# Kernel optimization log

Hardware: AMD Instinct MI355X
Metric: run time of the kernel (lower is better)

Reference implementation:

```python
import jax, jax.numpy as jnp
import numpy as np


def _bicubic_warp(img, dx, dy):
    """Faithful JAX port of Warp_Object.forward with flag='bicubic'.
    img: [B,C,H,W] float32; dx, dy: [B,1,H,W] pixel displacements.
    Replicates the original tile-order quirk: X/Y are repeated C times along
    dim0 (order c*B+b) while the image is flattened in b*C+c order.
    """
    B, C, H, W = img.shape
    Wm1 = jnp.float32(max(W - 1, 1))
    Hm1 = jnp.float32(max(H - 1, 1))
    xs = jnp.arange(W, dtype=jnp.float32)
    ys = jnp.arange(H, dtype=jnp.float32)
    Xg, Yg = jnp.meshgrid(xs, ys)          # [H,W]
    # normalized grid in [-1,1] as in forward()
    newX = 2.0 * (Xg[None] + dx[:, 0]) / Wm1 - 1.0   # [B,H,W]
    newY = 2.0 * (Yg[None] + dy[:, 0]) / Hm1 - 1.0
    # repeat over channels exactly like X.repeat([C,1,1,1]) (tile order)
    x_map = (jnp.tile(newX, (C, 1, 1)) + 1.0) * Wm1 / 2.0   # [B*C,H,W]
    y_map = (jnp.tile(newY, (C, 1, 1)) + 1.0) * Hm1 / 2.0

    x0 = jnp.floor(x_map)
    y0 = jnp.floor(y_map)
    tx = x_map - x0
    ty = y_map - y0

    def cubic_coeffs(t):
        cm1 = (-t ** 3 + 2.0 * t ** 2 - t) / 2.0
        c0 = (3.0 * t ** 3 - 5.0 * t ** 2 + 2.0) / 2.0
        c1 = (-3.0 * t ** 3 + 4.0 * t ** 2 + t) / 2.0
        c2 = 1.0 - (cm1 + c0 + c1)
        return (cm1, c0, c1, c2)

    cx = cubic_coeffs(tx)
    cy = cubic_coeffs(ty)

    x0i = x0.astype(jnp.int32)
    y0i = y0.astype(jnp.int32)
    xi = [jnp.clip(x0i + o, 0, W - 1) for o in (-1, 0, 1, 2)]
    yi = [jnp.clip(y0i + o, 0, H - 1) for o in (-1, 0, 1, 2)]

    flat = img.reshape(B * C, H, W)
    row = jnp.arange(B * C)[:, None, None]   # per-image base offset

    out = jnp.zeros_like(x_map)
    for j in range(4):            # 4 rows of the 4x4 bicubic stencil
        row_acc = jnp.zeros_like(x_map)
        for i in range(4):
            row_acc = row_acc + cx[i] * flat[row, yi[j], xi[i]]
        out = out + cy[j] * row_acc
    return out.reshape(B, C, H, W)


def setup_inputs() -> dict:
    key = jax.random.key(0)
    k1, k2, k3 = jax.random.split(key, 3)
    B, C, H, W = 4, 3, 512, 512
    input_image = jax.random.normal(k1, (B, C, H, W), dtype=jnp.float32)
    delta_x = jax.random.normal(k2, (B, 1, H, W), dtype=jnp.float32) * 1.5
    delta_y = jax.random.normal(k3, (B, 1, H, W), dtype=jnp.float32) * 1.5
    return {"input_image": input_image, "delta_x": delta_x, "delta_y": delta_y}


def reference(input_image, delta_x, delta_y):
    return _bicubic_warp(input_image, delta_x, delta_y)
```

## Files before the change

kernel.cpp:

```cpp
#include <hip/hip_runtime.h>


constexpr int B = 4, C = 3, H = 512, W = 512;
constexpr int HW = H * W;
constexpr int TH = 4;
constexpr int HALO_UP = 6, HALO_DN = 7;
constexpr int RS = TH + HALO_UP + HALO_DN;
constexpr int STRIDE = 516;
constexpr int NPOS = 4;
constexpr int NT = 512;
constexpr int NB = B * (H / TH);

typedef float f4 __attribute__((ext_vector_type(4)));
typedef f4 f4u __attribute__((aligned(4)));

__global__ __launch_bounds__(NT, 4)
void warp_bicubic_planes(const float* __restrict__ img,
                         const float* __restrict__ dxp,
                         const float* __restrict__ dyp,
                         float* __restrict__ out)
{
    __shared__ float tile[RS * STRIDE];

    int b   = blockIdx.x;
    int swz = (b & 7) * (NB / 8) + (b >> 3);
    int bd   = swz >> 7;
    int band = swz & 127;
    int yb   = band * TH;

    int tid  = threadIdx.x;
    int wave = tid >> 6;
    int ry   = wave >> 1;
    int half = wave & 1;
    int lane = tid & 63;
    int y    = yb + ry;
    int xbase = half * 256 + lane;

    const float* __restrict__ dxr = dxp + bd * HW + y * W + xbase;
    const float* __restrict__ dyr = dyp + bd * HW + y * W + xbase;
    float dxa[NPOS], dya[NPOS];
#pragma unroll
    for (int p = 0; p < NPOS; ++p) {
        dxa[p] = __builtin_nontemporal_load(dxr + 64 * p);
        dya[p] = __builtin_nontemporal_load(dyr + 64 * p);
    }

    float wx[NPOS][4];
    float cyw[NPOS][4];
    int   lbase[NPOS];
    unsigned relv[NPOS];
    int   sv[NPOS];
#pragma unroll
    for (int p = 0; p < NPOS; ++p) {
        int x = xbase + 64 * p;
        float xm = (float)x + dxa[p];
        float ym = (float)y + dya[p];
        float x0f = floorf(xm), y0f = floorf(ym);
        float tx = xm - x0f, ty = ym - y0f;
        int x0 = (int)x0f, y0 = (int)y0f;
        int s  = min(max(x0 - 1, 0), W - 4);
        sv[p] = s;

        float tx2 = tx * tx, tx3 = tx2 * tx;
        float cx0 = (-tx3 + 2.0f * tx2 - tx) * 0.5f;
        float cx1 = (3.0f * tx3 - 5.0f * tx2 + 2.0f) * 0.5f;
        float cx2 = (-3.0f * tx3 + 4.0f * tx2 + tx) * 0.5f;
        float cx3 = 1.0f - (cx0 + cx1 + cx2);

        float ty2 = ty * ty, ty3 = ty2 * ty;
        cyw[p][0] = (-ty3 + 2.0f * ty2 - ty) * 0.5f;
        cyw[p][1] = (3.0f * ty3 - 5.0f * ty2 + 2.0f) * 0.5f;
        cyw[p][2] = (-3.0f * ty3 + 4.0f * ty2 + ty) * 0.5f;
        cyw[p][3] = 1.0f - (cyw[p][0] + cyw[p][1] + cyw[p][2]);

        if (__builtin_expect(x0 >= 1 && x0 <= W - 3, 1)) {
            wx[p][0] = cx0; wx[p][1] = cx1; wx[p][2] = cx2; wx[p][3] = cx3;
        } else {
            float w0 = 0.f, w1 = 0.f, w2 = 0.f, w3 = 0.f;
            const float cxa[4] = {cx0, cx1, cx2, cx3};
#pragma unroll
            for (int o = 0; o < 4; ++o) {
                int xi = min(max(x0 - 1 + o, 0), W - 1);
                int e  = xi - s;
                float c = cxa[o];
                w0 += (e == 0) ? c : 0.f;
                w1 += (e == 1) ? c : 0.f;
                w2 += (e == 2) ? c : 0.f;
                w3 += (e == 3) ? c : 0.f;
            }
            wx[p][0] = w0; wx[p][1] = w1; wx[p][2] = w2; wx[p][3] = w3;
        }

        unsigned rel = (unsigned)(y0 - (yb - HALO_UP + 1));
        relv[p]  = rel;
        lbase[p] = (int)rel * STRIDE + s;
    }

#pragma unroll
    for (int c = 0; c < C; ++c) {
        int kp = bd + 4 * c;
        const float* __restrict__ plane = img + (size_t)kp * HW;

        if (c > 0) __syncthreads();
        for (int cc = tid; cc < RS * 128; cc += NT) {
            int r   = cc >> 7;
            int col = (cc & 127) << 2;
            int sr  = min(max(yb - HALO_UP + r, 0), H - 1);
            *(f4*)&tile[r * STRIDE + col] = *(const f4*)(plane + sr * W + col);
        }
        __syncthreads();

        float* __restrict__ orow = out + (size_t)kp * HW + y * W + xbase;
#pragma unroll
        for (int p = 0; p < NPOS; ++p) {
            float acc;
            if (__builtin_expect(relv[p] <= (unsigned)(RS - 4), 1)) {
                const float* rp = &tile[lbase[p]];
                float r0 = cyw[p][0] * (wx[p][0]*rp[0] + wx[p][1]*rp[1] + wx[p][2]*rp[2] + wx[p][3]*rp[3]);
                rp += STRIDE;
                float r1 = cyw[p][1] * (wx[p][0]*rp[0] + wx[p][1]*rp[1] + wx[p][2]*rp[2] + wx[p][3]*rp[3]);
                rp += STRIDE;
                float r2 = cyw[p][2] * (wx[p][0]*rp[0] + wx[p][1]*rp[1] + wx[p][2]*rp[2] + wx[p][3]*rp[3]);
                rp += STRIDE;
                float r3 = cyw[p][3] * (wx[p][0]*rp[0] + wx[p][1]*rp[1] + wx[p][2]*rp[2] + wx[p][3]*rp[3]);
                acc = (r0 + r1) + (r2 + r3);
            } else {
                int y0 = (int)relv[p] + (yb - HALO_UP + 1);
                acc = 0.f;
#pragma unroll
                for (int j = 0; j < 4; ++j) {
                    int yi = min(max(y0 - 1 + j, 0), H - 1);
                    f4 v = *(const f4u*)(plane + yi * W + sv[p]);
                    acc += cyw[p][j] * (wx[p][0]*v.x + wx[p][1]*v.y + wx[p][2]*v.z + wx[p][3]*v.w);
                }
            }
            __builtin_nontemporal_store(acc, orow + 64 * p);
        }
    }
}

extern "C" void kernel_launch(void* const* d_in, const int* in_sizes, int n_in,
                              void* d_out, int out_size, void* d_ws, size_t ws_size,
                              hipStream_t stream) {
    const float* img = (const float*)d_in[0];
    const float* dx  = (const float*)d_in[1];
    const float* dy  = (const float*)d_in[2];
    float* out = (float*)d_out;

    dim3 block(NT);
    dim3 grid(NB);
    hipLaunchKernelGGL(warp_bicubic_planes, grid, block, 0, stream,
                       img, dx, dy, out);
}
```

Baseline: 18.49 us.

## Split each row band into two x-halves with a narrower LDS tile

```diff
diff --git a/kernel.cpp b/kernel.cpp
--- a/kernel.cpp
+++ b/kernel.cpp
@@ -6,60 +6,60 @@
 constexpr int TH = 4;
 constexpr int HALO_UP = 6, HALO_DN = 7;
 constexpr int RS = TH + HALO_UP + HALO_DN;
-constexpr int STRIDE = 516;
-constexpr int NPOS = 4;
+constexpr int LST = 272;
+constexpr int NPOS = 2;
 constexpr int NT = 512;
-constexpr int NB = B * (H / TH);
+constexpr int NB = B * (H / TH) * 2;
 
 typedef float f4 __attribute__((ext_vector_type(4)));
 typedef f4 f4u __attribute__((aligned(4)));
 
-__global__ __launch_bounds__(NT, 4)
-void warp_bicubic_planes(const float* __restrict__ img,
+__global__ __launch_bounds__(NT, 8)
+void warp_bicubic_xsplit(const float* __restrict__ img,
                          const float* __restrict__ dxp,
                          const float* __restrict__ dyp,
                          float* __restrict__ out)
 {
-    __shared__ float tile[RS * STRIDE];
+    __shared__ float tile[RS * LST];
 
     int b   = blockIdx.x;
     int swz = (b & 7) * (NB / 8) + (b >> 3);
-    int bd   = swz >> 7;
-    int band = swz & 127;
+    int bd   = swz >> 8;
+    int band = (swz >> 1) & 127;
+    int half = swz & 1;
     int yb   = band * TH;
+    int xb   = half * 256;
+    int cb   = half ? 248 : 0;
 
     int tid  = threadIdx.x;
     int wave = tid >> 6;
     int ry   = wave >> 1;
-    int half = wave & 1;
+    int hw   = wave & 1;
     int lane = tid & 63;
     int y    = yb + ry;
-    int xbase = half * 256 + lane;
+    int xs   = xb + hw * 128 + lane;
+    int pixoff = y * W + xs;
 
-    const float* __restrict__ dxr = dxp + bd * HW + y * W + xbase;
-    const float* __restrict__ dyr = dyp + bd * HW + y * W + xbase;
     float dxa[NPOS], dya[NPOS];
 #pragma unroll
     for (int p = 0; p < NPOS; ++p) {
-        dxa[p] = __builtin_nontemporal_load(dxr + 64 * p);
-        dya[p] = __builtin_nontemporal_load(dyr + 64 * p);
+        dxa[p] = __builtin_nontemporal_load(dxp + bd * HW + pixoff + 64 * p);
+        dya[p] = __builtin_nontemporal_load(dyp + bd * HW + pixoff + 64 * p);
     }
 
     float wx[NPOS][4];
     float cyw[NPOS][4];
-    int   lbase[NPOS];
     unsigned relv[NPOS];
-    int   sv[NPOS];
+    unsigned lsv[NPOS];
 #pragma unroll
     for (int p = 0; p < NPOS; ++p) {
-        int x = xbase + 64 * p;
+        int x = xs + 64 * p;
         float xm = (float)x + dxa[p];
         float ym = (float)y + dya[p];
         float x0f = floorf(xm), y0f = floorf(ym);
         float tx = xm - x0f, ty = ym - y0f;
         int x0 = (int)x0f, y0 = (int)y0f;
         int s  = min(max(x0 - 1, 0), W - 4);
-        sv[p] = s;
 
         float tx2 = tx * tx, tx3 = tx2 * tx;
         float cx0 = (-tx3 + 2.0f * tx2 - tx) * 0.5f;
@@ -91,9 +91,8 @@
             wx[p][0] = w0; wx[p][1] = w1; wx[p][2] = w2; wx[p][3] = w3;
         }
 
-        unsigned rel = (unsigned)(y0 - (yb - HALO_UP + 1));
-        relv[p]  = rel;
-        lbase[p] = (int)rel * STRIDE + s;
+        relv[p] = (unsigned)(y0 - (yb - HALO_UP + 1));
+        lsv[p]  = (unsigned)(s - cb);
     }
 
 #pragma unroll
@@ -102,39 +101,42 @@
         const float* __restrict__ plane = img + (size_t)kp * HW;
 
         if (c > 0) __syncthreads();
-        for (int cc = tid; cc < RS * 128; cc += NT) {
-            int r   = cc >> 7;
-            int col = (cc & 127) << 2;
-            int sr  = min(max(yb - HALO_UP + r, 0), H - 1);
-            *(f4*)&tile[r * STRIDE + col] = *(const f4*)(plane + sr * W + col);
+        for (int cc = tid; cc < RS * (LST / 4); cc += NT) {
+            int r   = cc / (LST / 4);
+            int c4  = (cc - r * (LST / 4)) * 4;
+            int scol = min(cb + c4, W - 4);
+            int sr   = min(max(yb - HALO_UP + r, 0), H - 1);
+            *(f4*)&tile[r * LST + c4] = *(const f4*)(plane + sr * W + scol);
         }
         __syncthreads();
 
-        float* __restrict__ orow = out + (size_t)kp * HW + y * W + xbase;
+        float* __restrict__ obase = out + (size_t)kp * HW + pixoff;
 #pragma unroll
         for (int p = 0; p < NPOS; ++p) {
             float acc;
-            if (__builtin_expect(relv[p] <= (unsigned)(RS - 4), 1)) {
-                const float* rp = &tile[lbase[p]];
+            if (__builtin_expect(relv[p] <= (unsigned)(RS - 4) &&
+                                 lsv[p]  <= (unsigned)(LST - 4), 1)) {
+                const float* rp = &tile[relv[p] * LST + lsv[p]];
                 float r0 = cyw[p][0] * (wx[p][0]*rp[0] + wx[p][1]*rp[1] + wx[p][2]*rp[2] + wx[p][3]*rp[3]);
-                rp += STRIDE;
+                rp += LST;
                 float r1 = cyw[p][1] * (wx[p][0]*rp[0] + wx[p][1]*rp[1] + wx[p][2]*rp[2] + wx[p][3]*rp[3]);
-                rp += STRIDE;
+                rp += LST;
                 float r2 = cyw[p][2] * (wx[p][0]*rp[0] + wx[p][1]*rp[1] + wx[p][2]*rp[2] + wx[p][3]*rp[3]);
-                rp += STRIDE;
+                rp += LST;
                 float r3 = cyw[p][3] * (wx[p][0]*rp[0] + wx[p][1]*rp[1] + wx[p][2]*rp[2] + wx[p][3]*rp[3]);
                 acc = (r0 + r1) + (r2 + r3);
             } else {
                 int y0 = (int)relv[p] + (yb - HALO_UP + 1);
+                int s  = (int)lsv[p] + cb;
                 acc = 0.f;
 #pragma unroll
                 for (int j = 0; j < 4; ++j) {
                     int yi = min(max(y0 - 1 + j, 0), H - 1);
-                    f4 v = *(const f4u*)(plane + yi * W + sv[p]);
+                    f4 v = *(const f4u*)(plane + yi * W + s);
                     acc += cyw[p][j] * (wx[p][0]*v.x + wx[p][1]*v.y + wx[p][2]*v.z + wx[p][3]*v.w);
                 }
             }
-            __builtin_nontemporal_store(acc, orow + 64 * p);
+            __builtin_nontemporal_store(acc, obase + 64 * p);
         }
     }
 }
@@ -149,6 +151,6 @@
 
     dim3 block(NT);
     dim3 grid(NB);
-    hipLaunchKernelGGL(warp_bicubic_planes, grid, block, 0, stream,
+    hipLaunchKernelGGL(warp_bicubic_xsplit, grid, block, 0, stream,
                        img, dx, dy, out);
 }
```

Result: faster. 17.65 us (-4.6%).
